# Optimization experiments

Hardware: AMD Instinct MI355X
Metric: run time of the kernel (lower is better)

Reference implementation:

```python
import jax, jax.numpy as jnp
import numpy as np

IN_F, OUT_F = 4096, 4096
TOKENS = 8192


def setup_inputs() -> dict:
    key = jax.random.key(0)
    k = jax.random.split(key, 7)
    return {
        "x": jax.random.normal(k[0], (TOKENS, IN_F), dtype=jnp.float32),
        "weight_mu": jax.random.normal(k[1], (OUT_F, IN_F), dtype=jnp.float32) * 0.02,
        "weight_rho": jax.random.normal(k[2], (OUT_F, IN_F), dtype=jnp.float32) - 4.6,
        "bias_mu": jax.random.normal(k[3], (OUT_F,), dtype=jnp.float32) * 0.02,
        "bias_rho": jax.random.normal(k[4], (OUT_F,), dtype=jnp.float32) - 4.6,
        "eps_w": jax.random.normal(k[5], (OUT_F, IN_F), dtype=jnp.float32),
        "eps_b": jax.random.normal(k[6], (OUT_F,), dtype=jnp.float32),
    }


def reference(x, weight_mu, weight_rho, bias_mu, bias_rho, eps_w, eps_b):
    # Reparameterized sampling: W = mu + softplus(rho) * eps  (use_softplus=True)
    w = weight_mu + jax.nn.softplus(weight_rho) * eps_w      # [out, in]
    b = bias_mu + jax.nn.softplus(bias_rho) * eps_b          # [out]
    # F.linear: y = x @ W^T + b
    return jnp.einsum("ti,oi->to", x, w) + b
```

## Files before the change

kernel.cpp:

```cpp
#include <hip/hip_runtime.h>
#include <hip/hip_bf16.h>

#define TOKENS 8192
#define IN_F   4096
#define OUT_F  4096

#define BM 256
#define BN 256
#define BK 64
#define NT (IN_F / BK)

typedef __attribute__((ext_vector_type(8))) short bf16x8;
typedef __attribute__((ext_vector_type(4))) float f32x4;

static __device__ __forceinline__ unsigned short f2bf(float f) {
    union { float f; unsigned int u; } v;
    v.f = f;
    unsigned int r = v.u + 0x7fffu + ((v.u >> 16) & 1u);
    return (unsigned short)(r >> 16);
}

static __device__ __forceinline__ float softplus_fast(float x) {
    return __logf(1.0f + __expf(x));
}

#define XBLK 32768
#define WBLK 16384

__global__ __launch_bounds__(256) void prep_all_kernel(
        const float* __restrict__ x,
        const float* __restrict__ wmu,  const float* __restrict__ wrho,
        const float* __restrict__ epsw,
        const float* __restrict__ bmu,  const float* __restrict__ brho,
        const float* __restrict__ bepsb,
        __hip_bfloat16* __restrict__ xb, __hip_bfloat16* __restrict__ wb,
        float* __restrict__ bias) {
    const int b = blockIdx.x, t = threadIdx.x;
    if (b < XBLK) {
        const int i = b * 256 + t;
        float4 v = ((const float4*)x)[i];
        ushort4 o;
        o.x = f2bf(v.x); o.y = f2bf(v.y); o.z = f2bf(v.z); o.w = f2bf(v.w);
        ((ushort4*)xb)[i] = o;
    } else if (b < XBLK + WBLK) {
        const int i = (b - XBLK) * 256 + t;
        float4 m4 = ((const float4*)wmu)[i];
        float4 r4 = ((const float4*)wrho)[i];
        float4 e4 = ((const float4*)epsw)[i];
        ushort4 o;
        o.x = f2bf(m4.x + softplus_fast(r4.x) * e4.x);
        o.y = f2bf(m4.y + softplus_fast(r4.y) * e4.y);
        o.z = f2bf(m4.z + softplus_fast(r4.z) * e4.z);
        o.w = f2bf(m4.w + softplus_fast(r4.w) * e4.w);
        ((ushort4*)wb)[i] = o;
    } else {
        const int i = (b - XBLK - WBLK) * 256 + t;
        float4 m4 = ((const float4*)bmu)[i];
        float4 r4 = ((const float4*)brho)[i];
        float4 e4 = ((const float4*)bepsb)[i];
        float4 o;
        o.x = m4.x + softplus_fast(r4.x) * e4.x;
        o.y = m4.y + softplus_fast(r4.y) * e4.y;
        o.z = m4.z + softplus_fast(r4.z) * e4.z;
        o.w = m4.w + softplus_fast(r4.w) * e4.w;
        ((float4*)bias)[i] = o;
    }
}

__global__ __launch_bounds__(512, 2) void gemm_256_kernel(
        const __hip_bfloat16* __restrict__ Xb,
        const __hip_bfloat16* __restrict__ Wb,
        const float* __restrict__ bias,
        float* __restrict__ C) {
    __shared__ __align__(16) __hip_bfloat16 ldsA[2][2][BM * 32];
    __shared__ __align__(16) __hip_bfloat16 ldsB[2][2][BN * 32];

    const int tid  = threadIdx.x;
    const int lane = tid & 63;
    const int wave = tid >> 6;
    const int wm   = wave >> 2;
    const int wn   = wave & 3;
    const int fr   = lane & 15;
    const int quad = lane >> 4;

    const int rowBase = blockIdx.y * BM;
    const int colBase = blockIdx.x * BN;

    const int sRow = tid >> 2;
    const int sCol = ((tid & 3) ^ ((tid >> 3) & 3)) * 8;
    const __hip_bfloat16* gA = Xb + (size_t)(rowBase + sRow) * IN_F + sCol;
    const __hip_bfloat16* gB = Wb + (size_t)(colBase + sRow) * IN_F + sCol;
    const int dstE = tid * 8;

    const int chunk = quad ^ ((fr >> 1) & 3);
    const int aOffE = wm * 4096 + fr * 32 + chunk * 8;
    const int bOffE = wn * 2048 + fr * 32 + chunk * 8;

    auto stageA = [&](int slot, int kh, int kt) {
        const __hip_bfloat16* src = gA + (size_t)kt * BK + (size_t)kh * 32;
        __hip_bfloat16* dst = &ldsA[slot][kh][dstE];
        __builtin_amdgcn_global_load_lds(
            (const __attribute__((address_space(1))) void*)src,
            (__attribute__((address_space(3))) void*)dst, 16, 0, 0);
        __builtin_amdgcn_global_load_lds(
            (const __attribute__((address_space(1))) void*)(src + (size_t)128 * IN_F),
            (__attribute__((address_space(3))) void*)(dst + 4096), 16, 0, 0);
    };
    auto stageB = [&](int slot, int kh, int kt) {
        const __hip_bfloat16* src = gB + (size_t)kt * BK + (size_t)kh * 32;
        __hip_bfloat16* dst = &ldsB[slot][kh][dstE];
        __builtin_amdgcn_global_load_lds(
            (const __attribute__((address_space(1))) void*)src,
            (__attribute__((address_space(3))) void*)dst, 16, 0, 0);
        __builtin_amdgcn_global_load_lds(
            (const __attribute__((address_space(1))) void*)(src + (size_t)128 * IN_F),
            (__attribute__((address_space(3))) void*)(dst + 4096), 16, 0, 0);
    };

    f32x4 acc[8][4];
#pragma unroll
    for (int m = 0; m < 8; ++m)
#pragma unroll
        for (int n = 0; n < 4; ++n) acc[m][n] = (f32x4){0.f, 0.f, 0.f, 0.f};

    stageA(0, 0, 0);
    stageB(0, 0, 0);
    stageA(0, 1, 0);
    stageB(0, 1, 0);
    stageA(1, 0, 1);
    asm volatile("s_waitcnt vmcnt(6)" ::: "memory");
    __builtin_amdgcn_s_barrier();
    __builtin_amdgcn_sched_barrier(0);

    bf16x8 aR[4], bR[4];

    for (int t = 0; t < NT; ++t) {
        const int cs = t & 1, ns = cs ^ 1;
        const int t1 = (t + 1 < NT) ? (t + 1) : (NT - 1);
        const int t2 = (t + 2 < NT) ? (t + 2) : (NT - 1);
        const __hip_bfloat16* A0 = &ldsA[cs][0][0];
        const __hip_bfloat16* A1 = &ldsA[cs][1][0];
        const __hip_bfloat16* B0 = &ldsB[cs][0][0];
        const __hip_bfloat16* B1 = &ldsB[cs][1][0];

#pragma unroll
        for (int m = 0; m < 4; ++m) aR[m] = *(const bf16x8*)(A0 + aOffE + m * 512);
#pragma unroll
        for (int n = 0; n < 4; ++n) bR[n] = *(const bf16x8*)(B0 + bOffE + n * 512);
        stageB(ns, 0, t1);
        __builtin_amdgcn_s_barrier();
        asm volatile("s_waitcnt lgkmcnt(0)" ::: "memory");
        __builtin_amdgcn_s_setprio(1);
#pragma unroll
        for (int n = 0; n < 4; ++n)
#pragma unroll
            for (int m = 0; m < 4; ++m)
                acc[m][n] = __builtin_amdgcn_mfma_f32_16x16x32_bf16(aR[m], bR[n], acc[m][n], 0, 0, 0);
        __builtin_amdgcn_s_setprio(0);
        __builtin_amdgcn_s_barrier();

#pragma unroll
        for (int m = 0; m < 4; ++m) aR[m] = *(const bf16x8*)(A0 + aOffE + (m + 4) * 512);
        stageA(ns, 1, t1);
        __builtin_amdgcn_s_barrier();
        asm volatile("s_waitcnt lgkmcnt(0)" ::: "memory");
        __builtin_amdgcn_s_setprio(1);
#pragma unroll
        for (int n = 0; n < 4; ++n)
#pragma unroll
            for (int m = 0; m < 4; ++m)
                acc[m + 4][n] = __builtin_amdgcn_mfma_f32_16x16x32_bf16(aR[m], bR[n], acc[m + 4][n], 0, 0, 0);
        __builtin_amdgcn_s_setprio(0);
        asm volatile("s_waitcnt vmcnt(6)" ::: "memory");
        __builtin_amdgcn_s_barrier();
        __builtin_amdgcn_sched_barrier(0);

#pragma unroll
        for (int m = 0; m < 4; ++m) aR[m] = *(const bf16x8*)(A1 + aOffE + m * 512);
#pragma unroll
        for (int n = 0; n < 4; ++n) bR[n] = *(const bf16x8*)(B1 + bOffE + n * 512);
        stageB(ns, 1, t1);
        __builtin_amdgcn_s_barrier();
        asm volatile("s_waitcnt lgkmcnt(0)" ::: "memory");
        __builtin_amdgcn_s_setprio(1);
#pragma unroll
        for (int n = 0; n < 4; ++n)
#pragma unroll
            for (int m = 0; m < 4; ++m)
                acc[m][n] = __builtin_amdgcn_mfma_f32_16x16x32_bf16(aR[m], bR[n], acc[m][n], 0, 0, 0);
        __builtin_amdgcn_s_setprio(0);
        __builtin_amdgcn_s_barrier();

#pragma unroll
        for (int m = 0; m < 4; ++m) aR[m] = *(const bf16x8*)(A1 + aOffE + (m + 4) * 512);
        stageA(cs, 0, t2);
        __builtin_amdgcn_s_barrier();
        asm volatile("s_waitcnt lgkmcnt(0)" ::: "memory");
        __builtin_amdgcn_s_setprio(1);
#pragma unroll
        for (int n = 0; n < 4; ++n)
#pragma unroll
            for (int m = 0; m < 4; ++m)
                acc[m + 4][n] = __builtin_amdgcn_mfma_f32_16x16x32_bf16(aR[m], bR[n], acc[m + 4][n], 0, 0, 0);
        __builtin_amdgcn_s_setprio(0);
        asm volatile("s_waitcnt vmcnt(6)" ::: "memory");
        __builtin_amdgcn_s_barrier();
        __builtin_amdgcn_sched_barrier(0);
    }

#pragma unroll
    for (int n = 0; n < 4; ++n) {
        const int col = colBase + wn * 64 + n * 16 + fr;
        const float bv = bias[col];
#pragma unroll
        for (int m = 0; m < 8; ++m) {
            const int row = rowBase + wm * 128 + m * 16 + quad * 4;
#pragma unroll
            for (int r = 0; r < 4; ++r)
                C[(size_t)(row + r) * OUT_F + col] = acc[m][n][r] + bv;
        }
    }
}

extern "C" void kernel_launch(void* const* d_in, const int* in_sizes, int n_in,
                              void* d_out, int out_size, void* d_ws, size_t ws_size,
                              hipStream_t stream) {
    const float* x    = (const float*)d_in[0];
    const float* wmu  = (const float*)d_in[1];
    const float* wrho = (const float*)d_in[2];
    const float* bmu  = (const float*)d_in[3];
    const float* brho = (const float*)d_in[4];
    const float* epsw = (const float*)d_in[5];
    const float* epsb = (const float*)d_in[6];
    float* out = (float*)d_out;

    char* ws = (char*)d_ws;
    __hip_bfloat16* xb = (__hip_bfloat16*)ws;
    __hip_bfloat16* wb = (__hip_bfloat16*)(ws + (size_t)TOKENS * IN_F * 2);
    float* bias = (float*)(ws + (size_t)TOKENS * IN_F * 2 + (size_t)OUT_F * IN_F * 2);

    prep_all_kernel<<<XBLK + WBLK + 4, 256, 0, stream>>>(
        x, wmu, wrho, epsw, bmu, brho, epsb, xb, wb, bias);

    dim3 grid(OUT_F / BN, TOKENS / BM);
    gemm_256_kernel<<<grid, 512, 0, stream>>>(xb, wb, bias, out);
}
```

Baseline: 596.1 us.

## Switch GEMM to 32x32x16 MFMA tiles and add block-index swizzle

Replaces the 16x16x32 bf16 MFMA with 32x32x16 MFMA. This halves the number of LDS fragment reads per wave and the instruction count for the same work, and reworks the fragment addressing and epilogue indexing to match the 32x32 output layout. It also remaps block IDs so consecutive blocks share row and column tiles, aiming for better L2 reuse. The sched_barrier hints are removed, which gives the compiler more freedom and may change the interleaving of loads and MFMAs.

```diff
diff --git a/kernel.cpp b/kernel.cpp
--- a/kernel.cpp
+++ b/kernel.cpp
@@ -11,7 +11,7 @@
 #define NT (IN_F / BK)
 
 typedef __attribute__((ext_vector_type(8))) short bf16x8;
-typedef __attribute__((ext_vector_type(4))) float f32x4;
+typedef __attribute__((ext_vector_type(16))) float f32x16;
 
 static __device__ __forceinline__ unsigned short f2bf(float f) {
     union { float f; unsigned int u; } v;
@@ -80,21 +80,20 @@
     const int wave = tid >> 6;
     const int wm   = wave >> 2;
     const int wn   = wave & 3;
-    const int fr   = lane & 15;
-    const int quad = lane >> 4;
-
-    const int rowBase = blockIdx.y * BM;
-    const int colBase = blockIdx.x * BN;
+    const int rl   = lane & 31;
+    const int h    = lane >> 5;
+    const int xsw  = (rl >> 1) & 3;
+
+    int bid = blockIdx.y * 16 + blockIdx.x;
+    bid = (bid & 7) * 64 + (bid >> 3);
+    const int colBase = (bid & 15) * BN;
+    const int rowBase = (bid >> 4) * BM;
 
     const int sRow = tid >> 2;
     const int sCol = ((tid & 3) ^ ((tid >> 3) & 3)) * 8;
     const __hip_bfloat16* gA = Xb + (size_t)(rowBase + sRow) * IN_F + sCol;
     const __hip_bfloat16* gB = Wb + (size_t)(colBase + sRow) * IN_F + sCol;
     const int dstE = tid * 8;
-
-    const int chunk = quad ^ ((fr >> 1) & 3);
-    const int aOffE = wm * 4096 + fr * 32 + chunk * 8;
-    const int bOffE = wn * 2048 + fr * 32 + chunk * 8;
 
     auto stageA = [&](int slot, int kh, int kt) {
         const __hip_bfloat16* src = gA + (size_t)kt * BK + (size_t)kh * 32;
@@ -117,11 +116,18 @@
             (__attribute__((address_space(3))) void*)(dst + 4096), 16, 0, 0);
     };
 
-    f32x4 acc[8][4];
-#pragma unroll
-    for (int m = 0; m < 8; ++m)
-#pragma unroll
-        for (int n = 0; n < 4; ++n) acc[m][n] = (f32x4){0.f, 0.f, 0.f, 0.f};
+    f32x16 acc[4][2];
+#pragma unroll
+    for (int m = 0; m < 4; ++m)
+#pragma unroll
+        for (int n = 0; n < 2; ++n)
+#pragma unroll
+            for (int r = 0; r < 16; ++r) acc[m][n][r] = 0.f;
+
+    const int aBase = (wm * 128 + rl) * 32;
+    const int bBase = (wn * 64 + rl) * 32;
+    const int c0 = ((0 + h) ^ xsw) * 8;
+    const int c1 = ((2 + h) ^ xsw) * 8;
 
     stageA(0, 0, 0);
     stageB(0, 0, 0);
@@ -130,9 +136,8 @@
     stageA(1, 0, 1);
     asm volatile("s_waitcnt vmcnt(6)" ::: "memory");
     __builtin_amdgcn_s_barrier();
-    __builtin_amdgcn_sched_barrier(0);
-
-    bf16x8 aR[4], bR[4];
+
+    bf16x8 aR[2][2], bR[2][2];
 
     for (int t = 0; t < NT; ++t) {
         const int cs = t & 1, ns = cs ^ 1;
@@ -143,81 +148,105 @@
         const __hip_bfloat16* B0 = &ldsB[cs][0][0];
         const __hip_bfloat16* B1 = &ldsB[cs][1][0];
 
-#pragma unroll
-        for (int m = 0; m < 4; ++m) aR[m] = *(const bf16x8*)(A0 + aOffE + m * 512);
-#pragma unroll
-        for (int n = 0; n < 4; ++n) bR[n] = *(const bf16x8*)(B0 + bOffE + n * 512);
+        aR[0][0] = *(const bf16x8*)(A0 + aBase + c0);
+        aR[0][1] = *(const bf16x8*)(A0 + aBase + c1);
+        aR[1][0] = *(const bf16x8*)(A0 + aBase + 1024 + c0);
+        aR[1][1] = *(const bf16x8*)(A0 + aBase + 1024 + c1);
+        bR[0][0] = *(const bf16x8*)(B0 + bBase + c0);
+        bR[0][1] = *(const bf16x8*)(B0 + bBase + c1);
+        bR[1][0] = *(const bf16x8*)(B0 + bBase + 1024 + c0);
+        bR[1][1] = *(const bf16x8*)(B0 + bBase + 1024 + c1);
         stageB(ns, 0, t1);
         __builtin_amdgcn_s_barrier();
         asm volatile("s_waitcnt lgkmcnt(0)" ::: "memory");
         __builtin_amdgcn_s_setprio(1);
 #pragma unroll
-        for (int n = 0; n < 4; ++n)
-#pragma unroll
-            for (int m = 0; m < 4; ++m)
-                acc[m][n] = __builtin_amdgcn_mfma_f32_16x16x32_bf16(aR[m], bR[n], acc[m][n], 0, 0, 0);
-        __builtin_amdgcn_s_setprio(0);
-        __builtin_amdgcn_s_barrier();
-
-#pragma unroll
-        for (int m = 0; m < 4; ++m) aR[m] = *(const bf16x8*)(A0 + aOffE + (m + 4) * 512);
+        for (int s = 0; s < 2; ++s)
+#pragma unroll
+            for (int mt = 0; mt < 2; ++mt)
+#pragma unroll
+                for (int nt = 0; nt < 2; ++nt)
+                    acc[mt][nt] = __builtin_amdgcn_mfma_f32_32x32x16_bf16(
+                        aR[mt][s], bR[nt][s], acc[mt][nt], 0, 0, 0);
+        __builtin_amdgcn_s_setprio(0);
+        __builtin_amdgcn_s_barrier();
+
+        aR[0][0] = *(const bf16x8*)(A0 + aBase + 2048 + c0);
+        aR[0][1] = *(const bf16x8*)(A0 + aBase + 2048 + c1);
+        aR[1][0] = *(const bf16x8*)(A0 + aBase + 3072 + c0);
+        aR[1][1] = *(const bf16x8*)(A0 + aBase + 3072 + c1);
         stageA(ns, 1, t1);
         __builtin_amdgcn_s_barrier();
         asm volatile("s_waitcnt lgkmcnt(0)" ::: "memory");
         __builtin_amdgcn_s_setprio(1);
 #pragma unroll
-        for (int n = 0; n < 4; ++n)
-#pragma unroll
-            for (int m = 0; m < 4; ++m)
-                acc[m + 4][n] = __builtin_amdgcn_mfma_f32_16x16x32_bf16(aR[m], bR[n], acc[m + 4][n], 0, 0, 0);
+        for (int s = 0; s < 2; ++s)
+#pragma unroll
+            for (int mt = 0; mt < 2; ++mt)
+#pragma unroll
+                for (int nt = 0; nt < 2; ++nt)
+                    acc[mt + 2][nt] = __builtin_amdgcn_mfma_f32_32x32x16_bf16(
+                        aR[mt][s], bR[nt][s], acc[mt + 2][nt], 0, 0, 0);
         __builtin_amdgcn_s_setprio(0);
         asm volatile("s_waitcnt vmcnt(6)" ::: "memory");
         __builtin_amdgcn_s_barrier();
-        __builtin_amdgcn_sched_barrier(0);
-
-#pragma unroll
-        for (int m = 0; m < 4; ++m) aR[m] = *(const bf16x8*)(A1 + aOffE + m * 512);
-#pragma unroll
-        for (int n = 0; n < 4; ++n) bR[n] = *(const bf16x8*)(B1 + bOffE + n * 512);
+
+        aR[0][0] = *(const bf16x8*)(A1 + aBase + c0);
+        aR[0][1] = *(const bf16x8*)(A1 + aBase + c1);
+        aR[1][0] = *(const bf16x8*)(A1 + aBase + 1024 + c0);
+        aR[1][1] = *(const bf16x8*)(A1 + aBase + 1024 + c1);
+        bR[0][0] = *(const bf16x8*)(B1 + bBase + c0);
+        bR[0][1] = *(const bf16x8*)(B1 + bBase + c1);
+        bR[1][0] = *(const bf16x8*)(B1 + bBase + 1024 + c0);
+        bR[1][1] = *(const bf16x8*)(B1 + bBase + 1024 + c1);
         stageB(ns, 1, t1);
         __builtin_amdgcn_s_barrier();
         asm volatile("s_waitcnt lgkmcnt(0)" ::: "memory");
         __builtin_amdgcn_s_setprio(1);
 #pragma unroll
-        for (int n = 0; n < 4; ++n)
-#pragma unroll
-            for (int m = 0; m < 4; ++m)
-                acc[m][n] = __builtin_amdgcn_mfma_f32_16x16x32_bf16(aR[m], bR[n], acc[m][n], 0, 0, 0);
-        __builtin_amdgcn_s_setprio(0);
-        __builtin_amdgcn_s_barrier();
-
-#pragma unroll
-        for (int m = 0; m < 4; ++m) aR[m] = *(const bf16x8*)(A1 + aOffE + (m + 4) * 512);
+        for (int s = 0; s < 2; ++s)
+#pragma unroll
+            for (int mt = 0; mt < 2; ++mt)
+#pragma unroll
+                for (int nt = 0; nt < 2; ++nt)
+                    acc[mt][nt] = __builtin_amdgcn_mfma_f32_32x32x16_bf16(
+                        aR[mt][s], bR[nt][s], acc[mt][nt], 0, 0, 0);
+        __builtin_amdgcn_s_setprio(0);
+        __builtin_amdgcn_s_barrier();
+
+        aR[0][0] = *(const bf16x8*)(A1 + aBase + 2048 + c0);
+        aR[0][1] = *(const bf16x8*)(A1 + aBase + 2048 + c1);
+        aR[1][0] = *(const bf16x8*)(A1 + aBase + 3072 + c0);
+        aR[1][1] = *(const bf16x8*)(A1 + aBase + 3072 + c1);
         stageA(cs, 0, t2);
         __builtin_amdgcn_s_barrier();
         asm volatile("s_waitcnt lgkmcnt(0)" ::: "memory");
         __builtin_amdgcn_s_setprio(1);
 #pragma unroll
-        for (int n = 0; n < 4; ++n)
-#pragma unroll
-            for (int m = 0; m < 4; ++m)
-                acc[m + 4][n] = __builtin_amdgcn_mfma_f32_16x16x32_bf16(aR[m], bR[n], acc[m + 4][n], 0, 0, 0);
+        for (int s = 0; s < 2; ++s)
+#pragma unroll
+            for (int mt = 0; mt < 2; ++mt)
+#pragma unroll
+                for (int nt = 0; nt < 2; ++nt)
+                    acc[mt + 2][nt] = __builtin_amdgcn_mfma_f32_32x32x16_bf16(
+                        aR[mt][s], bR[nt][s], acc[mt + 2][nt], 0, 0, 0);
         __builtin_amdgcn_s_setprio(0);
         asm volatile("s_waitcnt vmcnt(6)" ::: "memory");
         __builtin_amdgcn_s_barrier();
-        __builtin_amdgcn_sched_barrier(0);
     }
 
 #pragma unroll
-    for (int n = 0; n < 4; ++n) {
-        const int col = colBase + wn * 64 + n * 16 + fr;
+    for (int nt = 0; nt < 2; ++nt) {
+        const int col = colBase + wn * 64 + nt * 32 + rl;
         const float bv = bias[col];
 #pragma unroll
-        for (int m = 0; m < 8; ++m) {
-            const int row = rowBase + wm * 128 + m * 16 + quad * 4;
-#pragma unroll
-            for (int r = 0; r < 4; ++r)
-                C[(size_t)(row + r) * OUT_F + col] = acc[m][n][r] + bv;
+        for (int mt = 0; mt < 4; ++mt) {
+            const int row0 = rowBase + wm * 128 + mt * 32 + h * 4;
+#pragma unroll
+            for (int r = 0; r < 16; ++r) {
+                const int row = row0 + (r & 3) + 8 * (r >> 2);
+                C[(size_t)row * OUT_F + col] = acc[mt][nt][r] + bv;
+            }
         }
     }
 }
```

After: 642.5 us. 7.8% more time.
